# Performance work log

Hardware: AMD Instinct MI355X
Metric: run time of the kernel (lower is better)

The kernel has to match this reference:

```python
import jax, jax.numpy as jnp
import numpy as np

B = 2097152
CXR, ECG, EHR = 15, 14, 13
TOTAL = CXR + ECG + EHR  # 42
LN_EPS = 1e-5


def setup_inputs() -> dict:
    key = jax.random.key(0)
    ks = jax.random.split(key, 40)
    f32 = jnp.float32
    inp = {
        "cxr_probs": jax.random.normal(ks[0], (B, CXR), dtype=f32),
        "ecg_probs": jax.random.normal(ks[1], (B, ECG), dtype=f32),
        "ehr_probs": jax.random.normal(ks[2], (B, EHR), dtype=f32),
    }
    for i, (name, E) in enumerate([("cxr", CXR), ("ecg", ECG), ("ehr", EHR)]):
        k0 = 3 + i * 8
        s_in = 1.0 / np.sqrt(E)
        s_kv = 1.0 / np.sqrt(TOTAL)
        inp[f"in_w_{name}"] = jax.random.normal(ks[k0], (3 * E, E), dtype=f32) * s_in
        inp[f"in_b_{name}"] = jnp.zeros((3 * E,), dtype=f32)
        inp[f"out_w_{name}"] = jax.random.normal(ks[k0 + 1], (E, E), dtype=f32) * s_in
        inp[f"out_b_{name}"] = jnp.zeros((E,), dtype=f32)
        inp[f"kv_w_{name}"] = jax.random.normal(ks[k0 + 2], (E, TOTAL), dtype=f32) * s_kv
        inp[f"kv_b_{name}"] = jax.random.normal(ks[k0 + 3], (E,), dtype=f32) * s_kv
        inp[f"ln_g_{name}"] = jnp.ones((E,), dtype=f32)
        inp[f"ln_b_{name}"] = jnp.zeros((E,), dtype=f32)
    return inp


def _branch(x, ctx, in_w, in_b, out_w, out_b, kv_w, kv_b, ln_g, ln_b):
    # x: [B, E], ctx: [B, 42]
    E = x.shape[-1]
    kv = ctx @ kv_w.T + kv_b                      # [B, E]
    # nn.MultiheadAttention with q_len = kv_len = 1: softmax over a single
    # key is identically 1, so attn_out == v_proj(kv) exactly.
    Wv, bv = in_w[2 * E:], in_b[2 * E:]
    v = kv @ Wv.T + bv                            # [B, E]
    attended = v @ out_w.T + out_b                # [B, E]
    y = x + attended
    mu = jnp.mean(y, axis=-1, keepdims=True)
    var = jnp.mean(jnp.square(y - mu), axis=-1, keepdims=True)
    return (y - mu) * jax.lax.rsqrt(var + LN_EPS) * ln_g + ln_b


def reference(cxr_probs, ecg_probs, ehr_probs,
              in_w_cxr, in_b_cxr, out_w_cxr, out_b_cxr, kv_w_cxr, kv_b_cxr, ln_g_cxr, ln_b_cxr,
              in_w_ecg, in_b_ecg, out_w_ecg, out_b_ecg, kv_w_ecg, kv_b_ecg, ln_g_ecg, ln_b_ecg,
              in_w_ehr, in_b_ehr, out_w_ehr, out_b_ehr, kv_w_ehr, kv_b_ehr, ln_g_ehr, ln_b_ehr):
    ctx = jnp.concatenate([cxr_probs, ecg_probs, ehr_probs], axis=1)  # [B, 42]
    cxr_out = _branch(cxr_probs, ctx, in_w_cxr, in_b_cxr, out_w_cxr, out_b_cxr,
                      kv_w_cxr, kv_b_cxr, ln_g_cxr, ln_b_cxr)
    ecg_out = _branch(ecg_probs, ctx, in_w_ecg, in_b_ecg, out_w_ecg, out_b_ecg,
                      kv_w_ecg, kv_b_ecg, ln_g_ecg, ln_b_ecg)
    ehr_out = _branch(ehr_probs, ctx, in_w_ehr, in_b_ehr, out_w_ehr, out_b_ehr,
                      kv_w_ehr, kv_b_ehr, ln_g_ehr, ln_b_ehr)
    return (cxr_out, ecg_out, ehr_out)
```

## Files before the change

### kernel.cpp

```cpp
#include <hip/hip_runtime.h>
#include <stdint.h>

constexpr int CXR = 15, ECG = 14, EHR = 13;
constexpr int TOTAL = 42;
constexpr int MPITCH = 44;
constexpr float LN_EPS = 1e-5f;

constexpr int WS_M    = 0;
constexpr int WS_B    = TOTAL * MPITCH;
constexpr int WS_G    = WS_B + TOTAL;
constexpr int WS_BETA = WS_G + TOTAL;
constexpr int WS_FRAG = 1976;

constexpr int WROWS = 64;
constexpr int S0F = 0, S1F = WROWS * CXR, S2F = S1F + WROWS * ECG;
constexpr int WC0 = WROWS * CXR / 4, WC1 = WROWS * ECG / 4, WC2 = WROWS * EHR / 4;
constexpr int STAGE_B = WROWS * TOTAL * 4;
constexpr int WORK_B  = WROWS * TOTAL * 4;
constexpr int ARENA_B = STAGE_B + WORK_B;

constexpr int GRID_BLOCKS = 1792;

typedef _Float16 half8 __attribute__((ext_vector_type(8)));
typedef float float4v __attribute__((ext_vector_type(4)));

struct FuseArgs {
    const float *in_w, *in_b, *out_w, *out_b, *kv_w, *kv_b, *ln_g, *ln_b;
    int E, R;
};

__global__ void fuse_weights_kernel(FuseArgs a0, FuseArgs a1, FuseArgs a2,
                                    float* __restrict__ ws) {
    FuseArgs a = (blockIdx.x == 0) ? a0 : (blockIdx.x == 1 ? a1 : a2);
    const int E = a.E, R = a.R;
    const int tid = threadIdx.x;

    __shared__ float T1[15 * 42];
    __shared__ float b1[15];

    for (int idx = tid; idx < E * TOTAL; idx += blockDim.x) {
        int i = idx / TOTAL, j = idx % TOTAL;
        float acc = 0.f;
        for (int k = 0; k < E; ++k)
            acc = fmaf(a.in_w[(2 * E + i) * E + k], a.kv_w[k * TOTAL + j], acc);
        T1[i * TOTAL + j] = acc;
    }
    if (tid < E) {
        float acc = a.in_b[2 * E + tid];
        for (int k = 0; k < E; ++k)
            acc = fmaf(a.in_w[(2 * E + tid) * E + k], a.kv_b[k], acc);
        b1[tid] = acc;
    }
    __syncthreads();

    for (int idx = tid; idx < E * MPITCH; idx += blockDim.x) {
        int i = idx / MPITCH, j = idx % MPITCH;
        float acc = 0.f;
        if (j < TOTAL)
            for (int k = 0; k < E; ++k)
                acc = fmaf(a.out_w[i * E + k], T1[k * TOTAL + j], acc);
        ws[WS_M + (R + i) * MPITCH + j] = acc;
    }
    if (tid < E) {
        float acc = a.out_b[tid];
        for (int k = 0; k < E; ++k)
            acc = fmaf(a.out_w[tid * E + k], b1[k], acc);
        ws[WS_B + R + tid]    = acc;
        ws[WS_G + R + tid]    = a.ln_g[tid];
        ws[WS_BETA + R + tid] = a.ln_b[tid];
    }
}

__global__ void fuse_frags_kernel(float* __restrict__ ws) {
    const int tid = threadIdx.x;
    if (tid >= 384) return;
    const int l = tid & 63, nt = tid >> 6;
    const int m = nt >> 1, t = nt & 1;
    const int j = l & 15;
    const int k0 = t * 32 + 8 * (l >> 4);
    const int offm = (m == 0) ? 0 : (m == 1 ? CXR : CXR + ECG);
    const int Em   = (m == 0) ? CXR : (m == 1 ? ECG : EHR);
    half8 h;
#pragma unroll
    for (int i = 0; i < 8; ++i) {
        int k = k0 + i;
        float v = 0.f;
        if (j < Em) {
            int glob = offm + j;
            if (k < TOTAL) {
                v = ws[WS_M + glob * MPITCH + k];
                if (k == glob) v += 1.f;
            } else if (k == TOTAL) {
                v = ws[WS_B + glob];
            }
        }
        h[i] = (_Float16)v;
    }
    ((half8*)(ws + WS_FRAG))[nt * 64 + l] = h;
}

template <int CH>
__device__ __forceinline__ void stage_seg(const float* __restrict__ g,
                                          float* lds_seg_base, int lane) {
#pragma unroll
    for (int it = 0; it < (CH + 63) / 64; ++it) {
        int idx = lane + it * 64;
        if (idx < CH) {
            const __attribute__((address_space(1))) void* src =
                (const __attribute__((address_space(1))) void*)
                    ((const char*)g + (size_t)idx * 16);
            __attribute__((address_space(3))) void* dst =
                (__attribute__((address_space(3))) void*)
                    ((char*)lds_seg_base + it * 1024);
            __builtin_amdgcn_global_load_lds(src, dst, 16, 0, 0);
        }
    }
}

__global__ __launch_bounds__(64) void cmca_main(
        const float* __restrict__ cxr, const float* __restrict__ ecg,
        const float* __restrict__ ehr, const float* __restrict__ ws,
        float* __restrict__ out_cxr, float* __restrict__ out_ecg,
        float* __restrict__ out_ehr, int NT) {
    __shared__ __align__(16) char arena[ARENA_B];
    float* stg = (float*)arena;
    char*  fb  = arena + STAGE_B;
    float* wk  = (float*)(arena + STAGE_B);

    const int lane = threadIdx.x;
    const int h = lane >> 4, b15 = lane & 15;

    const half8* fr = (const half8*)(ws + WS_FRAG);
    half8 wf[3][2];
#pragma unroll
    for (int m = 0; m < 3; ++m)
#pragma unroll
        for (int t = 0; t < 2; ++t) wf[m][t] = fr[(m * 2 + t) * 64 + lane];

    constexpr int Earr[3]  = {CXR, ECG, EHR};
    constexpr int OFFa[3]  = {0, CXR, CXR + ECG};
    float gg[3][4], bb[3][4];
#pragma unroll
    for (int m = 0; m < 3; ++m)
#pragma unroll
        for (int r = 0; r < 4; ++r) {
            int j = 4 * h + r;
            bool v = j < Earr[m];
            gg[m][r] = v ? ws[WS_G + OFFa[m] + j] : 0.f;
            bb[m][r] = v ? ws[WS_BETA + OFFa[m] + j] : 0.f;
        }

    const int t0 = blockIdx.x;
    stage_seg<WC0>(cxr + (size_t)t0 * (WROWS * CXR), stg + S0F, lane);
    stage_seg<WC1>(ecg + (size_t)t0 * (WROWS * ECG), stg + S1F, lane);
    stage_seg<WC2>(ehr + (size_t)t0 * (WROWS * EHR), stg + S2F, lane);
    asm volatile("s_waitcnt vmcnt(0)" ::: "memory");

    for (int t = t0; t < NT; t += GRID_BLOCKS) {
        float x[TOTAL];
#pragma unroll
        for (int j = 0; j < CXR; ++j) x[j] = stg[S0F + lane * CXR + j];
#pragma unroll
        for (int j = 0; j < ECG; ++j) x[CXR + j] = stg[S1F + lane * ECG + j];
#pragma unroll
        for (int j = 0; j < EHR; ++j) x[CXR + ECG + j] = stg[S2F + lane * EHR + j];
        asm volatile("s_waitcnt lgkmcnt(0)" ::: "memory");
        __builtin_amdgcn_sched_barrier(0);

        const int tn = t + GRID_BLOCKS;
        const bool more = tn < NT;
        if (more) {
            stage_seg<WC0>(cxr + (size_t)tn * (WROWS * CXR), stg + S0F, lane);
            stage_seg<WC1>(ecg + (size_t)tn * (WROWS * ECG), stg + S1F, lane);
            stage_seg<WC2>(ehr + (size_t)tn * (WROWS * EHR), stg + S2F, lane);
        }

        const int swz = (lane & 7) << 4;
#pragma unroll
        for (int j = 0; j < 6; ++j) {
            half8 h8;
#pragma unroll
            for (int e = 0; e < 8; ++e) {
                int k = j * 8 + e;
                float v = (k < TOTAL) ? x[k] : (k == TOTAL ? 1.f : 0.f);
                h8[e] = (_Float16)v;
            }
            *(half8*)(fb + lane * 128 + ((j * 16) ^ swz)) = h8;
        }
        *(float4v*)(fb + lane * 128 + (96 ^ swz))  = float4v{0.f, 0.f, 0.f, 0.f};
        *(float4v*)(fb + lane * 128 + (112 ^ swz)) = float4v{0.f, 0.f, 0.f, 0.f};

        half8 xf[4][2];
#pragma unroll
        for (int n = 0; n < 4; ++n) {
            int row = n * 16 + b15;
            int rsw = (row & 7) << 4;
#pragma unroll
            for (int t2 = 0; t2 < 2; ++t2)
                xf[n][t2] = *(const half8*)(fb + row * 128 +
                                            ((t2 * 64 + h * 16) ^ rsw));
        }

        float4v acc[3][4];
#pragma unroll
        for (int m = 0; m < 3; ++m)
#pragma unroll
            for (int n = 0; n < 4; ++n) acc[m][n] = float4v{0.f, 0.f, 0.f, 0.f};
#pragma unroll
        for (int t2 = 0; t2 < 2; ++t2)
#pragma unroll
            for (int m = 0; m < 3; ++m)
#pragma unroll
                for (int n = 0; n < 4; ++n)
                    acc[m][n] = __builtin_amdgcn_mfma_f32_16x16x32_f16(
                        wf[m][t2], xf[n][t2], acc[m][n], 0, 0, 0);

#pragma unroll
        for (int n = 0; n < 4; ++n) {
            int brow = n * 16 + b15;
#pragma unroll
            for (int m = 0; m < 3; ++m) {
                constexpr int SEGF[3] = {S0F, S1F, S2F};
                const int E = Earr[m];
                const float invE = 1.0f / E;
                const float PAD = (float)(16 - E);
                float s = acc[m][n][0] + acc[m][n][1] + acc[m][n][2] + acc[m][n][3];
                s += __shfl_xor(s, 16, 64);
                s += __shfl_xor(s, 32, 64);
                float mu = s * invE;
                float q = 0.f;
#pragma unroll
                for (int r = 0; r < 4; ++r) {
                    float d = acc[m][n][r] - mu;
                    q = fmaf(d, d, q);
                }
                q += __shfl_xor(q, 16, 64);
                q += __shfl_xor(q, 32, 64);
                float var = (q - PAD * mu * mu) * invE;
                float rs = rsqrtf(var + LN_EPS);
#pragma unroll
                for (int r = 0; r < 4; ++r) {
                    int j = 4 * h + r;
                    if (j < E) {
                        float nv = (acc[m][n][r] - mu) * rs;
                        wk[SEGF[m] + brow * E + j] = fmaf(nv, gg[m][r], bb[m][r]);
                    }
                }
            }
        }

        const float4v* w4 = (const float4v*)wk;
        float4v* o0 = (float4v*)(out_cxr + (size_t)t * (WROWS * CXR));
        float4v* o1 = (float4v*)(out_ecg + (size_t)t * (WROWS * ECG));
        float4v* o2 = (float4v*)(out_ehr + (size_t)t * (WROWS * EHR));
#pragma unroll
        for (int it = 0; it < 4; ++it) {
            int idx = lane + it * 64;
            if (idx < WC0) o0[idx] = w4[idx];
        }
#pragma unroll
        for (int it = 0; it < 4; ++it) {
            int idx = lane + it * 64;
            if (idx < WC1) o1[idx] = w4[WC0 + idx];
        }
#pragma unroll
        for (int it = 0; it < 4; ++it) {
            int idx = lane + it * 64;
            if (idx < WC2) o2[idx] = w4[WC0 + WC1 + idx];
        }

        if (more) {
            asm volatile("s_waitcnt vmcnt(12)" ::: "memory");
            __builtin_amdgcn_sched_barrier(0);
        }
    }
}

extern "C" void kernel_launch(void* const* d_in, const int* in_sizes, int n_in,
                              void* d_out, int out_size, void* d_ws, size_t ws_size,
                              hipStream_t stream) {
    const float* cxr = (const float*)d_in[0];
    const float* ecg = (const float*)d_in[1];
    const float* ehr = (const float*)d_in[2];
    float* ws = (float*)d_ws;
    float* out = (float*)d_out;

    const size_t Bn = (size_t)in_sizes[0] / CXR;

    auto mk = [&](int base, int E, int R) {
        FuseArgs a;
        a.in_w  = (const float*)d_in[base + 0];
        a.in_b  = (const float*)d_in[base + 1];
        a.out_w = (const float*)d_in[base + 2];
        a.out_b = (const float*)d_in[base + 3];
        a.kv_w  = (const float*)d_in[base + 4];
        a.kv_b  = (const float*)d_in[base + 5];
        a.ln_g  = (const float*)d_in[base + 6];
        a.ln_b  = (const float*)d_in[base + 7];
        a.E = E; a.R = R;
        return a;
    };
    FuseArgs a0 = mk(3, CXR, 0);
    FuseArgs a1 = mk(11, ECG, CXR);
    FuseArgs a2 = mk(19, EHR, CXR + ECG);

    fuse_weights_kernel<<<3, 256, 0, stream>>>(a0, a1, a2, ws);
    fuse_frags_kernel<<<1, 384, 0, stream>>>(ws);

    const int NT = (int)(Bn / WROWS);
    cmca_main<<<GRID_BLOCKS, 64, 0, stream>>>(cxr, ecg, ehr, ws,
                                              out,
                                              out + Bn * CXR,
                                              out + Bn * (CXR + ECG), NT);
}
```

Before: 162.2 us.

## Replace persistent pipelined loop with one-tile-per-wave grid and direct stores

Drops the persistent 1792-block loop with software-pipelined double staging and launches one block of two waves per pair of 64-row tiles. Activation fragments are now read straight from the staged LDS into half8 registers instead of going through a swizzled f16 LDS buffer. LayerNorm uses a single-pass sum and sum-of-squares, and results are written directly to global memory with scattered per-element stores rather than staged through LDS for coalesced float4 writes. This trades cross-iteration load/compute overlap for more resident waves and less LDS traffic, at the risk of uncoalesced output stores and lost prefetch overlap.

Measured after the change: 188.6 us. 1.16x slower.

```diff
diff --git a/kernel.cpp b/kernel.cpp
--- a/kernel.cpp
+++ b/kernel.cpp
@@ -14,12 +14,8 @@
 
 constexpr int WROWS = 64;
 constexpr int S0F = 0, S1F = WROWS * CXR, S2F = S1F + WROWS * ECG;
+constexpr int ARENA_F = S2F + WROWS * EHR;
 constexpr int WC0 = WROWS * CXR / 4, WC1 = WROWS * ECG / 4, WC2 = WROWS * EHR / 4;
-constexpr int STAGE_B = WROWS * TOTAL * 4;
-constexpr int WORK_B  = WROWS * TOTAL * 4;
-constexpr int ARENA_B = STAGE_B + WORK_B;
-
-constexpr int GRID_BLOCKS = 1792;
 
 typedef _Float16 half8 __attribute__((ext_vector_type(8)));
 typedef float float4v __attribute__((ext_vector_type(4)));
@@ -117,18 +113,21 @@
     }
 }
 
-__global__ __launch_bounds__(64) void cmca_main(
+__global__ __launch_bounds__(128) void cmca_main(
         const float* __restrict__ cxr, const float* __restrict__ ecg,
         const float* __restrict__ ehr, const float* __restrict__ ws,
         float* __restrict__ out_cxr, float* __restrict__ out_ecg,
-        float* __restrict__ out_ehr, int NT) {
-    __shared__ __align__(16) char arena[ARENA_B];
-    float* stg = (float*)arena;
-    char*  fb  = arena + STAGE_B;
-    float* wk  = (float*)(arena + STAGE_B);
-
-    const int lane = threadIdx.x;
+        float* __restrict__ out_ehr) {
+    __shared__ __align__(16) float sbuf[2 * ARENA_F];
+    const int tid = threadIdx.x;
+    const int w = tid >> 6, lane = tid & 63;
+    float* stg = sbuf + w * ARENA_F;
+    const size_t gw = (size_t)blockIdx.x * 2 + w;
     const int h = lane >> 4, b15 = lane & 15;
+
+    stage_seg<WC0>(cxr + gw * (size_t)(WROWS * CXR), stg + S0F, lane);
+    stage_seg<WC1>(ecg + gw * (size_t)(WROWS * ECG), stg + S1F, lane);
+    stage_seg<WC2>(ehr + gw * (size_t)(WROWS * EHR), stg + S2F, lane);
 
     const half8* fr = (const half8*)(ws + WS_FRAG);
     half8 wf[3][2];
@@ -137,8 +136,8 @@
 #pragma unroll
         for (int t = 0; t < 2; ++t) wf[m][t] = fr[(m * 2 + t) * 64 + lane];
 
-    constexpr int Earr[3]  = {CXR, ECG, EHR};
-    constexpr int OFFa[3]  = {0, CXR, CXR + ECG};
+    constexpr int Earr[3] = {CXR, ECG, EHR};
+    constexpr int OFFa[3] = {0, CXR, CXR + ECG};
     float gg[3][4], bb[3][4];
 #pragma unroll
     for (int m = 0; m < 3; ++m)
@@ -150,128 +149,82 @@
             bb[m][r] = v ? ws[WS_BETA + OFFa[m] + j] : 0.f;
         }
 
-    const int t0 = blockIdx.x;
-    stage_seg<WC0>(cxr + (size_t)t0 * (WROWS * CXR), stg + S0F, lane);
-    stage_seg<WC1>(ecg + (size_t)t0 * (WROWS * ECG), stg + S1F, lane);
-    stage_seg<WC2>(ehr + (size_t)t0 * (WROWS * EHR), stg + S2F, lane);
     asm volatile("s_waitcnt vmcnt(0)" ::: "memory");
-
-    for (int t = t0; t < NT; t += GRID_BLOCKS) {
-        float x[TOTAL];
-#pragma unroll
-        for (int j = 0; j < CXR; ++j) x[j] = stg[S0F + lane * CXR + j];
-#pragma unroll
-        for (int j = 0; j < ECG; ++j) x[CXR + j] = stg[S1F + lane * ECG + j];
-#pragma unroll
-        for (int j = 0; j < EHR; ++j) x[CXR + ECG + j] = stg[S2F + lane * EHR + j];
-        asm volatile("s_waitcnt lgkmcnt(0)" ::: "memory");
-        __builtin_amdgcn_sched_barrier(0);
-
-        const int tn = t + GRID_BLOCKS;
-        const bool more = tn < NT;
-        if (more) {
-            stage_seg<WC0>(cxr + (size_t)tn * (WROWS * CXR), stg + S0F, lane);
-            stage_seg<WC1>(ecg + (size_t)tn * (WROWS * ECG), stg + S1F, lane);
-            stage_seg<WC2>(ehr + (size_t)tn * (WROWS * EHR), stg + S2F, lane);
-        }
-
-        const int swz = (lane & 7) << 4;
-#pragma unroll
-        for (int j = 0; j < 6; ++j) {
-            half8 h8;
-#pragma unroll
-            for (int e = 0; e < 8; ++e) {
-                int k = j * 8 + e;
-                float v = (k < TOTAL) ? x[k] : (k == TOTAL ? 1.f : 0.f);
-                h8[e] = (_Float16)v;
-            }
-            *(half8*)(fb + lane * 128 + ((j * 16) ^ swz)) = h8;
-        }
-        *(float4v*)(fb + lane * 128 + (96 ^ swz))  = float4v{0.f, 0.f, 0.f, 0.f};
-        *(float4v*)(fb + lane * 128 + (112 ^ swz)) = float4v{0.f, 0.f, 0.f, 0.f};
-
-        half8 xf[4][2];
+    __builtin_amdgcn_sched_barrier(0);
+
+    const int k0a = 8 * h;
+    const int k0b = 32 + 8 * h;
+
+    float4v acc[3][4];
+#pragma unroll
+    for (int m = 0; m < 3; ++m)
+#pragma unroll
+        for (int n = 0; n < 4; ++n) acc[m][n] = float4v{0.f, 0.f, 0.f, 0.f};
+
+#pragma unroll
+    for (int n = 0; n < 4; ++n) {
+        const int batch = n * 16 + b15;
+        const int o15 = batch * 15;
+        const int o14 = S1F - 15 + batch * 14;
+        const int o13 = S2F - 29 + batch * 13;
+
+        half8 x0, x1;
+#pragma unroll
+        for (int e = 0; e < 8; ++e) {
+            int k = k0a + e;
+            int off = o15 + k;
+            off = (k >= 15) ? (o14 + k) : off;
+            off = (k >= 29) ? (o13 + k) : off;
+            x0[e] = (_Float16)stg[off];
+        }
+#pragma unroll
+        for (int e = 0; e < 8; ++e) {
+            int k = k0b + e;
+            float v = (k == TOTAL) ? 1.f : 0.f;
+            if (k < TOTAL) v = stg[o13 + k];
+            x1[e] = (_Float16)v;
+        }
+#pragma unroll
+        for (int m = 0; m < 3; ++m) {
+            acc[m][n] = __builtin_amdgcn_mfma_f32_16x16x32_f16(
+                wf[m][0], x0, acc[m][n], 0, 0, 0);
+            acc[m][n] = __builtin_amdgcn_mfma_f32_16x16x32_f16(
+                wf[m][1], x1, acc[m][n], 0, 0, 0);
+        }
+    }
+
+    float* const outs[3] = {
+        out_cxr + gw * (size_t)(WROWS * CXR),
+        out_ecg + gw * (size_t)(WROWS * ECG),
+        out_ehr + gw * (size_t)(WROWS * EHR)};
+#pragma unroll
+    for (int m = 0; m < 3; ++m) {
+        const int E = Earr[m];
+        const float invE = 1.0f / E;
+        float* ob = outs[m];
 #pragma unroll
         for (int n = 0; n < 4; ++n) {
-            int row = n * 16 + b15;
-            int rsw = (row & 7) << 4;
-#pragma unroll
-            for (int t2 = 0; t2 < 2; ++t2)
-                xf[n][t2] = *(const half8*)(fb + row * 128 +
-                                            ((t2 * 64 + h * 16) ^ rsw));
-        }
-
-        float4v acc[3][4];
-#pragma unroll
-        for (int m = 0; m < 3; ++m)
-#pragma unroll
-            for (int n = 0; n < 4; ++n) acc[m][n] = float4v{0.f, 0.f, 0.f, 0.f};
-#pragma unroll
-        for (int t2 = 0; t2 < 2; ++t2)
-#pragma unroll
-            for (int m = 0; m < 3; ++m)
-#pragma unroll
-                for (int n = 0; n < 4; ++n)
-                    acc[m][n] = __builtin_amdgcn_mfma_f32_16x16x32_f16(
-                        wf[m][t2], xf[n][t2], acc[m][n], 0, 0, 0);
-
-#pragma unroll
-        for (int n = 0; n < 4; ++n) {
-            int brow = n * 16 + b15;
-#pragma unroll
-            for (int m = 0; m < 3; ++m) {
-                constexpr int SEGF[3] = {S0F, S1F, S2F};
-                const int E = Earr[m];
-                const float invE = 1.0f / E;
-                const float PAD = (float)(16 - E);
-                float s = acc[m][n][0] + acc[m][n][1] + acc[m][n][2] + acc[m][n][3];
-                s += __shfl_xor(s, 16, 64);
-                s += __shfl_xor(s, 32, 64);
-                float mu = s * invE;
-                float q = 0.f;
-#pragma unroll
-                for (int r = 0; r < 4; ++r) {
-                    float d = acc[m][n][r] - mu;
-                    q = fmaf(d, d, q);
-                }
-                q += __shfl_xor(q, 16, 64);
-                q += __shfl_xor(q, 32, 64);
-                float var = (q - PAD * mu * mu) * invE;
-                float rs = rsqrtf(var + LN_EPS);
-#pragma unroll
-                for (int r = 0; r < 4; ++r) {
-                    int j = 4 * h + r;
-                    if (j < E) {
-                        float nv = (acc[m][n][r] - mu) * rs;
-                        wk[SEGF[m] + brow * E + j] = fmaf(nv, gg[m][r], bb[m][r]);
-                    }
+            float s  = acc[m][n][0] + acc[m][n][1] + acc[m][n][2] + acc[m][n][3];
+            float ss = acc[m][n][0] * acc[m][n][0];
+            ss = fmaf(acc[m][n][1], acc[m][n][1], ss);
+            ss = fmaf(acc[m][n][2], acc[m][n][2], ss);
+            ss = fmaf(acc[m][n][3], acc[m][n][3], ss);
+            s  += __shfl_xor(s, 16, 64);
+            ss += __shfl_xor(ss, 16, 64);
+            s  += __shfl_xor(s, 32, 64);
+            ss += __shfl_xor(ss, 32, 64);
+            float mu  = s * invE;
+            float var = fmaf(ss, invE, -mu * mu);
+            float rs  = rsqrtf(var + LN_EPS);
+            const int row = n * 16 + b15;
+#pragma unroll
+            for (int r = 0; r < 4; ++r) {
+                int j = 4 * h + r;
+                if (j < E) {
+                    float nv = (acc[m][n][r] - mu) * rs;
+                    ob[(size_t)row * E + j] = fmaf(nv, gg[m][r], bb[m][r]);
                 }
             }
-        }
-
-        const float4v* w4 = (const float4v*)wk;
-        float4v* o0 = (float4v*)(out_cxr + (size_t)t * (WROWS * CXR));
-        float4v* o1 = (float4v*)(out_ecg + (size_t)t * (WROWS * ECG));
-        float4v* o2 = (float4v*)(out_ehr + (size_t)t * (WROWS * EHR));
-#pragma unroll
-        for (int it = 0; it < 4; ++it) {
-            int idx = lane + it * 64;
-            if (idx < WC0) o0[idx] = w4[idx];
-        }
-#pragma unroll
-        for (int it = 0; it < 4; ++it) {
-            int idx = lane + it * 64;
-            if (idx < WC1) o1[idx] = w4[WC0 + idx];
-        }
-#pragma unroll
-        for (int it = 0; it < 4; ++it) {
-            int idx = lane + it * 64;
-            if (idx < WC2) o2[idx] = w4[WC0 + WC1 + idx];
-        }
-
-        if (more) {
-            asm volatile("s_waitcnt vmcnt(12)" ::: "memory");
-            __builtin_amdgcn_sched_barrier(0);
         }
     }
 }
@@ -307,9 +260,9 @@
     fuse_weights_kernel<<<3, 256, 0, stream>>>(a0, a1, a2, ws);
     fuse_frags_kernel<<<1, 384, 0, stream>>>(ws);
 
-    const int NT = (int)(Bn / WROWS);
-    cmca_main<<<GRID_BLOCKS, 64, 0, stream>>>(cxr, ecg, ehr, ws,
-                                              out,
-                                              out + Bn * CXR,
-                                              out + Bn * (CXR + ECG), NT);
-}
+    const int nblocks = (int)(Bn / (WROWS * 2));
+    cmca_main<<<nblocks, 128, 0, stream>>>(cxr, ecg, ehr, ws,
+                                           out,
+                                           out + Bn * CXR,
+                                           out + Bn * (CXR + ECG));
+}
```
